# Performance work log

Measured on AMD Instinct MI355X. Metric: run time of the kernel, lower is better.

The kernel has to match this reference:

```python
import jax, jax.numpy as jnp
import numpy as np

EPS = 1e-12  # torch F.normalize eps

def _l2norm(v, axis):
    n = jnp.sqrt(jnp.sum(v * v, axis=axis, keepdims=True))
    return v / jnp.maximum(n, EPS)

def setup_inputs() -> dict:
    key = jax.random.key(0)
    k1, k2 = jax.random.split(key)
    B, N, D, K = 8, 2048, 128, 64
    x = jax.random.normal(k1, (B, N, D), dtype=jnp.float32)
    std1 = 1.0 / np.sqrt(K * D)
    centroids = jax.random.uniform(k2, (K, D), dtype=jnp.float32, minval=-std1, maxval=std1)
    return {"x": x, "centroids": centroids}

def reference(x, centroids):
    # x: [B, N, D], centroids: [K, D]
    B, N, D = x.shape
    K = centroids.shape[0]
    xn = _l2norm(x, axis=-1)                       # descriptor-wise L2 normalize
    res = xn[:, :, None, :] - centroids[None, None]  # [B, N, K, D]
    dist = jnp.sum(res * res, axis=-1)             # [B, N, K] squared distances
    assign = jax.nn.softmax(dist, axis=-1)         # softmax over clusters (NOTE: positive distances, as in source)
    vlad = jnp.einsum('bnk,bnkd->bkd', assign, res)  # weighted residual sum over N
    vlad = _l2norm(vlad, axis=2)                   # intra-normalization per cluster
    vlad = vlad.reshape(B, K * D)
    vlad = _l2norm(vlad, axis=1)                   # global L2 normalize
    return vlad
```

## Files before the change

### kernel.cpp

```cpp
#include <hip/hip_runtime.h>
#include <math.h>

#define BB 8
#define NN 2048
#define DD 128
#define KK 64
#define PP 128
#define NPB (NN / PP)

__global__ __launch_bounds__(256, 4) void netvlad_k1(
    const float* __restrict__ x, const float* __restrict__ cent,
    float* __restrict__ part_acc, float* __restrict__ part_sA)
{
    const int b    = blockIdx.x >> 7;
    const int p    = blockIdx.x & 127;
    const int t    = threadIdx.x;
    const int kq   = t >> 3;
    const int pr   = t & 7;
    const int dbase = pr * 16;
    const int wave = t >> 6;
    const int lane = t & 63;
    const int half = (t >> 5) & 1;
    const int hl   = t & 31;

    __shared__ float xn[8][DD];
    __shared__ float eL[8][KK];
    __shared__ float rsum[8];

    int off[4];
    #pragma unroll
    for (int jj = 0; jj < 4; ++jj) off[jj] = dbase + (((jj + pr) & 3) << 2);

    float4 cA[4], cB[4];
    float cn2a = 0.f, cn2b = 0.f;
    #pragma unroll
    for (int jj = 0; jj < 4; ++jj) {
        cA[jj] = *(const float4*)(cent + (2 * kq) * DD + off[jj]);
        cB[jj] = *(const float4*)(cent + (2 * kq + 1) * DD + off[jj]);
        cn2a += cA[jj].x*cA[jj].x + cA[jj].y*cA[jj].y + cA[jj].z*cA[jj].z + cA[jj].w*cA[jj].w;
        cn2b += cB[jj].x*cB[jj].x + cB[jj].y*cB[jj].y + cB[jj].z*cB[jj].z + cB[jj].w*cB[jj].w;
    }
    #pragma unroll
    for (int m = 1; m < 8; m <<= 1) {
        cn2a += __shfl_xor(cn2a, m);
        cn2b += __shfl_xor(cn2b, m);
    }

    float4 acc0[4], acc1[4];
    #pragma unroll
    for (int jj = 0; jj < 4; ++jj) {
        acc0[jj] = make_float4(0.f, 0.f, 0.f, 0.f);
        acc1[jj] = make_float4(0.f, 0.f, 0.f, 0.f);
    }
    float sA0 = 0.f, sA1 = 0.f;

    const float* xb = x + ((size_t)b * NN + (size_t)p * NPB) * DD;

    for (int it = 0; it < NPB / 8; ++it) {
        __syncthreads();

        {
            const int i = wave * 2 + half;
            const float* xp = xb + (size_t)(it * 8 + i) * DD + hl * 4;
            float4 v = *(const float4*)xp;
            float ss = v.x*v.x + v.y*v.y + v.z*v.z + v.w*v.w;
            #pragma unroll
            for (int m = 1; m < 32; m <<= 1) ss += __shfl_xor(ss, m);
            const float rn = 1.0f / fmaxf(sqrtf(ss), 1e-12f);
            *(float4*)(&xn[i][hl * 4]) = make_float4(v.x*rn, v.y*rn, v.z*rn, v.w*rn);
        }
        __syncthreads();

        float e0[8], e1[8];
        #pragma unroll
        for (int i = 0; i < 8; ++i) {
            float S0 = 0.f, S1 = 0.f;
            #pragma unroll
            for (int jj = 0; jj < 4; ++jj) {
                float4 v = *(const float4*)(&xn[i][off[jj]]);
                S0 += v.x*cA[jj].x + v.y*cA[jj].y + v.z*cA[jj].z + v.w*cA[jj].w;
                S1 += v.x*cB[jj].x + v.y*cB[jj].y + v.z*cB[jj].z + v.w*cB[jj].w;
            }
            #pragma unroll
            for (int m = 1; m < 8; m <<= 1) {
                S0 += __shfl_xor(S0, m);
                S1 += __shfl_xor(S1, m);
            }
            e0[i] = __expf(cn2a - 2.f * S0);
            e1[i] = __expf(cn2b - 2.f * S1);
            if (pr == 0) *(float2*)(&eL[i][2 * kq]) = make_float2(e0[i], e1[i]);
        }
        __syncthreads();

        #pragma unroll
        for (int rep = 0; rep < 2; ++rep) {
            const int i = wave * 2 + rep;
            float e = eL[i][lane];
            #pragma unroll
            for (int m = 1; m < 64; m <<= 1) e += __shfl_xor(e, m);
            if (lane == 0) rsum[i] = 1.0f / e;
        }
        __syncthreads();

        #pragma unroll
        for (int i = 0; i < 8; ++i) {
            const float r = rsum[i];
            const float a0 = e0[i] * r, a1 = e1[i] * r;
            sA0 += a0; sA1 += a1;
            #pragma unroll
            for (int jj = 0; jj < 4; ++jj) {
                float4 v = *(const float4*)(&xn[i][off[jj]]);
                acc0[jj].x += a0*v.x; acc0[jj].y += a0*v.y; acc0[jj].z += a0*v.z; acc0[jj].w += a0*v.w;
                acc1[jj].x += a1*v.x; acc1[jj].y += a1*v.y; acc1[jj].z += a1*v.z; acc1[jj].w += a1*v.w;
            }
        }
    }

    const size_t base = (size_t)(b * PP + p) * KK * DD;
    #pragma unroll
    for (int jj = 0; jj < 4; ++jj) {
        *(float4*)(part_acc + base + (2 * kq) * DD + off[jj])     = acc0[jj];
        *(float4*)(part_acc + base + (2 * kq + 1) * DD + off[jj]) = acc1[jj];
    }
    if (pr == 0) {
        part_sA[(b * PP + p) * KK + 2 * kq]     = sA0;
        part_sA[(b * PP + p) * KK + 2 * kq + 1] = sA1;
    }
}

__global__ __launch_bounds__(128) void netvlad_k2(
    const float* __restrict__ cent, const float* __restrict__ part_acc,
    const float* __restrict__ part_sA, float* __restrict__ out)
{
    const int b  = blockIdx.x >> 6;
    const int k  = blockIdx.x & 63;
    const int t  = threadIdx.x;
    const int d4 = t & 31;
    const int ps = t >> 5;

    __shared__ float sAL[2];
    {
        float sA = part_sA[(b * PP + t) * KK + k];
        #pragma unroll
        for (int m = 1; m < 64; m <<= 1) sA += __shfl_xor(sA, m);
        if ((t & 63) == 0) sAL[t >> 6] = sA;
    }

    float4 acc = make_float4(0.f, 0.f, 0.f, 0.f);
    const float* base = part_acc + ((size_t)(b * PP) * KK + k) * DD + d4 * 4;
    #pragma unroll 8
    for (int pp = 0; pp < 32; ++pp) {
        const float4 v = *(const float4*)(base + (size_t)(ps * 32 + pp) * KK * DD);
        acc.x += v.x; acc.y += v.y; acc.z += v.z; acc.w += v.w;
    }

    __shared__ float4 red[4][32];
    red[ps][d4] = acc;
    __syncthreads();
    const float sAt = sAL[0] + sAL[1];

    if (t < 32) {
        float4 v = red[0][t];
        #pragma unroll
        for (int s = 1; s < 4; ++s) {
            v.x += red[s][t].x; v.y += red[s][t].y;
            v.z += red[s][t].z; v.w += red[s][t].w;
        }
        const float4 c = *(const float4*)(cent + k * DD + t * 4);
        v.x -= c.x * sAt; v.y -= c.y * sAt; v.z -= c.z * sAt; v.w -= c.w * sAt;

        float ss = v.x*v.x + v.y*v.y + v.z*v.z + v.w*v.w;
        #pragma unroll
        for (int m = 1; m < 32; m <<= 1) ss += __shfl_xor(ss, m);
        const float rn = 0.125f / fmaxf(sqrtf(ss), 1e-12f);
        v.x *= rn; v.y *= rn; v.z *= rn; v.w *= rn;
        *(float4*)(out + ((size_t)b * KK + k) * DD + t * 4) = v;
    }
}

extern "C" void kernel_launch(void* const* d_in, const int* in_sizes, int n_in,
                              void* d_out, int out_size, void* d_ws, size_t ws_size,
                              hipStream_t stream) {
    const float* x    = (const float*)d_in[0];
    const float* cent = (const float*)d_in[1];
    float* out = (float*)d_out;

    char* ws = (char*)d_ws;
    float* part_sA  = (float*)ws;
    float* part_acc = (float*)(ws + (1 << 19));

    netvlad_k1<<<dim3(BB * PP), dim3(256), 0, stream>>>(x, cent, part_acc, part_sA);
    netvlad_k2<<<dim3(BB * KK), dim3(128), 0, stream>>>(cent, part_acc, part_sA, out);
}
```

Before: 98.87 us.

## Halve partial blocks, give each thread four clusters, use DPP reductions

```diff
diff --git a/kernel.cpp b/kernel.cpp
--- a/kernel.cpp
+++ b/kernel.cpp
@@ -5,126 +5,139 @@
 #define NN 2048
 #define DD 128
 #define KK 64
-#define PP 128
+#define PP 64
 #define NPB (NN / PP)
+
+template <int CTRL>
+__device__ __forceinline__ float dppadd(float x) {
+    return x + __int_as_float(__builtin_amdgcn_update_dpp(
+        0, __float_as_int(x), CTRL, 0xF, 0xF, true));
+}
+__device__ __forceinline__ float row16sum(float x) {
+    x = dppadd<0xB1>(x);
+    x = dppadd<0x4E>(x);
+    x = dppadd<0x141>(x);
+    x = dppadd<0x140>(x);
+    return x;
+}
+__device__ __forceinline__ float sum32(float x) {
+    x = row16sum(x);
+    return x + __int_as_float(
+        __builtin_amdgcn_ds_swizzle(__float_as_int(x), 0x401F));
+}
+__device__ __forceinline__ float dot4(float4 a, float4 b) {
+    return a.x*b.x + a.y*b.y + a.z*b.z + a.w*b.w;
+}
 
 __global__ __launch_bounds__(256, 4) void netvlad_k1(
     const float* __restrict__ x, const float* __restrict__ cent,
     float* __restrict__ part_acc, float* __restrict__ part_sA)
 {
-    const int b    = blockIdx.x >> 7;
-    const int p    = blockIdx.x & 127;
+    const int b    = blockIdx.x >> 6;
+    const int p    = blockIdx.x & 63;
     const int t    = threadIdx.x;
-    const int kq   = t >> 3;
-    const int pr   = t & 7;
-    const int dbase = pr * 16;
+    const int kq   = t >> 4;
+    const int pr   = t & 15;
     const int wave = t >> 6;
     const int lane = t & 63;
     const int half = (t >> 5) & 1;
     const int hl   = t & 31;
 
-    __shared__ float xn[8][DD];
-    __shared__ float eL[8][KK];
-    __shared__ float rsum[8];
-
-    int off[4];
+    __shared__ float4 xn4[8][32];
+    __shared__ float  eL[4][KK];
+    __shared__ __align__(16) float rsum[4];
+
+    float4 c0[4], c1[4];
+    float cn2[4];
     #pragma unroll
-    for (int jj = 0; jj < 4; ++jj) off[jj] = dbase + (((jj + pr) & 3) << 2);
-
-    float4 cA[4], cB[4];
-    float cn2a = 0.f, cn2b = 0.f;
+    for (int kk = 0; kk < 4; ++kk) {
+        const int k = kq * 4 + kk;
+        c0[kk] = *(const float4*)(cent + k * DD + pr * 4);
+        c1[kk] = *(const float4*)(cent + k * DD + 64 + pr * 4);
+        cn2[kk] = row16sum(dot4(c0[kk], c0[kk]) + dot4(c1[kk], c1[kk]));
+    }
+
+    float4 acc0[4], acc1[4];
+    float sA[4];
     #pragma unroll
-    for (int jj = 0; jj < 4; ++jj) {
-        cA[jj] = *(const float4*)(cent + (2 * kq) * DD + off[jj]);
-        cB[jj] = *(const float4*)(cent + (2 * kq + 1) * DD + off[jj]);
-        cn2a += cA[jj].x*cA[jj].x + cA[jj].y*cA[jj].y + cA[jj].z*cA[jj].z + cA[jj].w*cA[jj].w;
-        cn2b += cB[jj].x*cB[jj].x + cB[jj].y*cB[jj].y + cB[jj].z*cB[jj].z + cB[jj].w*cB[jj].w;
-    }
-    #pragma unroll
-    for (int m = 1; m < 8; m <<= 1) {
-        cn2a += __shfl_xor(cn2a, m);
-        cn2b += __shfl_xor(cn2b, m);
-    }
-
-    float4 acc0[4], acc1[4];
-    #pragma unroll
-    for (int jj = 0; jj < 4; ++jj) {
-        acc0[jj] = make_float4(0.f, 0.f, 0.f, 0.f);
-        acc1[jj] = make_float4(0.f, 0.f, 0.f, 0.f);
-    }
-    float sA0 = 0.f, sA1 = 0.f;
+    for (int kk = 0; kk < 4; ++kk) {
+        acc0[kk] = make_float4(0.f, 0.f, 0.f, 0.f);
+        acc1[kk] = make_float4(0.f, 0.f, 0.f, 0.f);
+        sA[kk] = 0.f;
+    }
 
     const float* xb = x + ((size_t)b * NN + (size_t)p * NPB) * DD;
 
-    for (int it = 0; it < NPB / 8; ++it) {
+    for (int outer = 0; outer < NPB / 8; ++outer) {
         __syncthreads();
 
         {
-            const int i = wave * 2 + half;
-            const float* xp = xb + (size_t)(it * 8 + i) * DD + hl * 4;
+            const int r = (wave << 1) | half;
+            const float* xp = xb + (size_t)(outer * 8 + r) * DD + hl * 4;
             float4 v = *(const float4*)xp;
-            float ss = v.x*v.x + v.y*v.y + v.z*v.z + v.w*v.w;
-            #pragma unroll
-            for (int m = 1; m < 32; m <<= 1) ss += __shfl_xor(ss, m);
+            float ss = sum32(v.x*v.x + v.y*v.y + v.z*v.z + v.w*v.w);
             const float rn = 1.0f / fmaxf(sqrtf(ss), 1e-12f);
-            *(float4*)(&xn[i][hl * 4]) = make_float4(v.x*rn, v.y*rn, v.z*rn, v.w*rn);
+            xn4[r][hl] = make_float4(v.x*rn, v.y*rn, v.z*rn, v.w*rn);
         }
         __syncthreads();
 
-        float e0[8], e1[8];
-        #pragma unroll
-        for (int i = 0; i < 8; ++i) {
-            float S0 = 0.f, S1 = 0.f;
+        for (int sub = 0; sub < 2; ++sub) {
+            const int r0 = sub * 4;
+
+            float e[4][4];
             #pragma unroll
-            for (int jj = 0; jj < 4; ++jj) {
-                float4 v = *(const float4*)(&xn[i][off[jj]]);
-                S0 += v.x*cA[jj].x + v.y*cA[jj].y + v.z*cA[jj].z + v.w*cA[jj].w;
-                S1 += v.x*cB[jj].x + v.y*cB[jj].y + v.z*cB[jj].z + v.w*cB[jj].w;
+            for (int i = 0; i < 4; ++i) {
+                const float4 u0 = xn4[r0 + i][pr];
+                const float4 u1 = xn4[r0 + i][16 + pr];
+                #pragma unroll
+                for (int kk = 0; kk < 4; ++kk) {
+                    float S = dot4(u0, c0[kk]) + dot4(u1, c1[kk]);
+                    S = row16sum(S);
+                    e[i][kk] = __expf(cn2[kk] - 2.0f * S);
+                }
+                if (pr == 0)
+                    *(float4*)(&eL[i][kq * 4]) =
+                        make_float4(e[i][0], e[i][1], e[i][2], e[i][3]);
             }
+            __syncthreads();
+
+            {
+                const float2 ev = *(const float2*)(&eL[wave][(lane & 31) * 2]);
+                const float s = sum32(ev.x + ev.y);
+                if (lane == 0) rsum[wave] = 1.0f / s;
+            }
+            __syncthreads();
+
+            const float4 rv = *(const float4*)rsum;
             #pragma unroll
-            for (int m = 1; m < 8; m <<= 1) {
-                S0 += __shfl_xor(S0, m);
-                S1 += __shfl_xor(S1, m);
-            }
-            e0[i] = __expf(cn2a - 2.f * S0);
-            e1[i] = __expf(cn2b - 2.f * S1);
-            if (pr == 0) *(float2*)(&eL[i][2 * kq]) = make_float2(e0[i], e1[i]);
-        }
-        __syncthreads();
-
-        #pragma unroll
-        for (int rep = 0; rep < 2; ++rep) {
-            const int i = wave * 2 + rep;
-            float e = eL[i][lane];
-            #pragma unroll
-            for (int m = 1; m < 64; m <<= 1) e += __shfl_xor(e, m);
-            if (lane == 0) rsum[i] = 1.0f / e;
-        }
-        __syncthreads();
-
-        #pragma unroll
-        for (int i = 0; i < 8; ++i) {
-            const float r = rsum[i];
-            const float a0 = e0[i] * r, a1 = e1[i] * r;
-            sA0 += a0; sA1 += a1;
-            #pragma unroll
-            for (int jj = 0; jj < 4; ++jj) {
-                float4 v = *(const float4*)(&xn[i][off[jj]]);
-                acc0[jj].x += a0*v.x; acc0[jj].y += a0*v.y; acc0[jj].z += a0*v.z; acc0[jj].w += a0*v.w;
-                acc1[jj].x += a1*v.x; acc1[jj].y += a1*v.y; acc1[jj].z += a1*v.z; acc1[jj].w += a1*v.w;
+            for (int i = 0; i < 4; ++i) {
+                const float4 u0 = xn4[r0 + i][pr];
+                const float4 u1 = xn4[r0 + i][16 + pr];
+                const float ri = (&rv.x)[i];
+                #pragma unroll
+                for (int kk = 0; kk < 4; ++kk) {
+                    const float a = e[i][kk] * ri;
+                    sA[kk] += a;
+                    acc0[kk].x += a*u0.x; acc0[kk].y += a*u0.y;
+                    acc0[kk].z += a*u0.z; acc0[kk].w += a*u0.w;
+                    acc1[kk].x += a*u1.x; acc1[kk].y += a*u1.y;
+                    acc1[kk].z += a*u1.z; acc1[kk].w += a*u1.w;
+                }
             }
         }
     }
 
+    if (pr == 0) {
+        #pragma unroll
+        for (int kk = 0; kk < 4; ++kk)
+            part_sA[((size_t)b * KK + kq * 4 + kk) * PP + p] = sA[kk];
+    }
     const size_t base = (size_t)(b * PP + p) * KK * DD;
     #pragma unroll
-    for (int jj = 0; jj < 4; ++jj) {
-        *(float4*)(part_acc + base + (2 * kq) * DD + off[jj])     = acc0[jj];
-        *(float4*)(part_acc + base + (2 * kq + 1) * DD + off[jj]) = acc1[jj];
-    }
-    if (pr == 0) {
-        part_sA[(b * PP + p) * KK + 2 * kq]     = sA0;
-        part_sA[(b * PP + p) * KK + 2 * kq + 1] = sA1;
+    for (int kk = 0; kk < 4; ++kk) {
+        const int k = kq * 4 + kk;
+        *(float4*)(part_acc + base + k * DD + pr * 4)      = acc0[kk];
+        *(float4*)(part_acc + base + k * DD + 64 + pr * 4) = acc1[kk];
     }
 }
 
@@ -138,26 +151,26 @@
     const int d4 = t & 31;
     const int ps = t >> 5;
 
-    __shared__ float sAL[2];
-    {
-        float sA = part_sA[(b * PP + t) * KK + k];
+    __shared__ float sAL;
+    if (t < 64) {
+        float sA = part_sA[((size_t)b * KK + k) * PP + t];
         #pragma unroll
         for (int m = 1; m < 64; m <<= 1) sA += __shfl_xor(sA, m);
-        if ((t & 63) == 0) sAL[t >> 6] = sA;
+        if (t == 0) sAL = sA;
     }
 
     float4 acc = make_float4(0.f, 0.f, 0.f, 0.f);
-    const float* base = part_acc + ((size_t)(b * PP) * KK + k) * DD + d4 * 4;
+    const float* basep = part_acc + ((size_t)(b * PP) * KK + k) * DD + d4 * 4;
     #pragma unroll 8
-    for (int pp = 0; pp < 32; ++pp) {
-        const float4 v = *(const float4*)(base + (size_t)(ps * 32 + pp) * KK * DD);
+    for (int pp = 0; pp < 16; ++pp) {
+        const float4 v = *(const float4*)(basep + (size_t)(ps * 16 + pp) * KK * DD);
         acc.x += v.x; acc.y += v.y; acc.z += v.z; acc.w += v.w;
     }
 
     __shared__ float4 red[4][32];
     red[ps][d4] = acc;
     __syncthreads();
-    const float sAt = sAL[0] + sAL[1];
+    const float sAt = sAL;
 
     if (t < 32) {
         float4 v = red[0][t];
@@ -187,7 +200,7 @@
 
     char* ws = (char*)d_ws;
     float* part_sA  = (float*)ws;
-    float* part_acc = (float*)(ws + (1 << 19));
+    float* part_acc = (float*)(ws + (1 << 18));
 
     netvlad_k1<<<dim3(BB * PP), dim3(256), 0, stream>>>(x, cent, part_acc, part_sA);
     netvlad_k2<<<dim3(BB * KK), dim3(128), 0, stream>>>(cent, part_acc, part_sA, out);
```

New measurement: 111.2 us. 12.5% more time.
